# Performance work log

Measured on AMD Instinct MI355X. Metric: run time of the kernel, lower is better.

## Reference

```python
import jax, jax.numpy as jnp
import numpy as np

N, E, IN, H, C = 50000, 800000, 128, 256, 2
EPS = 1e-5


def setup_inputs() -> dict:
    key = jax.random.key(0)
    ks = jax.random.split(key, 12)
    inp = {
        "x": jax.random.normal(ks[0], (N, IN), jnp.float32),
        "edge_index": jax.random.randint(ks[1], (2, E), 0, N, jnp.int32),
        "w_nei0": jax.random.normal(ks[2], (IN, H), jnp.float32) * 0.05,
        "w_root0": jax.random.normal(ks[3], (IN, H), jnp.float32) * 0.05,
        "b0": jnp.zeros((H,), jnp.float32),
        "w_nei": jax.random.normal(ks[4], (2, H, H), jnp.float32) * 0.05,
        "w_root": jax.random.normal(ks[5], (2, H, H), jnp.float32) * 0.05,
        "b": jnp.zeros((2, H), jnp.float32),
        "bn_gamma": jnp.ones((3, H), jnp.float32),
        "bn_beta": jnp.zeros((3, H), jnp.float32),
        "bn_mean": jax.random.normal(ks[6], (3, H), jnp.float32) * 0.05,
        "bn_var": jnp.ones((3, H), jnp.float32),
        "w1": jax.random.normal(ks[7], (H, H // 2), jnp.float32) * 0.05,
        "b1": jnp.zeros((H // 2,), jnp.float32),
        "w2": jax.random.normal(ks[8], (H // 2, C), jnp.float32) * 0.05,
        "b2": jnp.zeros((C,), jnp.float32),
    }
    return inp


def _mean_aggregate(h, src, dst, inv_deg):
    # gather source-node features, scatter-sum to destinations, divide by degree
    agg = jax.ops.segment_sum(h[src], dst, num_segments=N)  # (N, d)
    return agg * inv_deg[:, None]


def _forward(x, edge_index, w_nei0, w_root0, b0, w_nei, w_root, b,
             bn_gamma, bn_beta, bn_mean, bn_var, w1, b1, w2, b2):
    src, dst = edge_index[0], edge_index[1]
    deg = jax.ops.segment_sum(jnp.ones((E,), x.dtype), dst, num_segments=N)
    inv_deg = 1.0 / jnp.maximum(deg, 1.0)

    h = x
    wn_list = [w_nei0, w_nei[0], w_nei[1]]
    wr_list = [w_root0, w_root[0], w_root[1]]
    bias_list = [b0, b[0], b[1]]
    for i in range(3):
        mean_nb = _mean_aggregate(h, src, dst, inv_deg)          # (N, d_in)
        h = mean_nb @ wn_list[i] + bias_list[i] + h @ wr_list[i]  # SAGEConv
        # BatchNorm1d (eval: running stats) + ReLU; dropout is identity in eval
        h = (h - bn_mean[i]) * jax.lax.rsqrt(bn_var[i] + EPS) * bn_gamma[i] + bn_beta[i]
        h = jax.nn.relu(h)

    h = jax.nn.relu(h @ w1 + b1)
    logits = h @ w2 + b2
    return jax.nn.log_softmax(logits, axis=1)


def reference(x, edge_index, w_nei0, w_root0, b0, w_nei, w_root, b,
              bn_gamma, bn_beta, bn_mean, bn_var, w1, b1, w2, b2):
    return _forward(x, edge_index, w_nei0, w_root0, b0, w_nei, w_root, b,
                    bn_gamma, bn_beta, bn_mean, bn_var, w1, b1, w2, b2)
```

## Files before the change

kernel.cpp:

```cpp
#include <hip/hip_runtime.h>
#include <hip/hip_fp16.h>

#define N_NODES 50000
#define N_EDGES 800000
#define DIM_IN 128
#define DIM_H 256

typedef _Float16 f16;
typedef _Float16 half8 __attribute__((ext_vector_type(8)));
typedef _Float16 f16x4 __attribute__((ext_vector_type(4)));
typedef _Float16 f16x2 __attribute__((ext_vector_type(2)));
typedef float f32x4 __attribute__((ext_vector_type(4)));
typedef unsigned int u32;

__device__ __forceinline__ void gload_lds16(const void* g, void* l) {
    __builtin_amdgcn_global_load_lds(
        (const __attribute__((address_space(1))) u32*)g,
        (__attribute__((address_space(3))) u32*)l,
        16, 0, 0);
}


__global__ void k_deg(const int* __restrict__ dst, int* __restrict__ deg) {
    int i = blockIdx.x * 256 + threadIdx.x;
    if (i < N_EDGES) atomicAdd(&deg[dst[i]], 1);
}

__global__ void k_scan1(const int* __restrict__ deg, int* __restrict__ row_start,
                        int* __restrict__ partials) {
    __shared__ int sm[256];
    int t = threadIdx.x;
    int i = blockIdx.x * 256 + t;
    int v = (i < N_NODES) ? deg[i] : 0;
    sm[t] = v;
    __syncthreads();
    for (int ofs = 1; ofs < 256; ofs <<= 1) {
        int add = (t >= ofs) ? sm[t - ofs] : 0;
        __syncthreads();
        sm[t] += add;
        __syncthreads();
    }
    if (i < N_NODES) row_start[i] = sm[t] - v;
    if (t == 255) partials[blockIdx.x] = sm[255];
}

__global__ void k_scan2(const int* __restrict__ partials, int* __restrict__ pscan, int nblk) {
    __shared__ int sm[256];
    int t = threadIdx.x;
    int v = (t < nblk) ? partials[t] : 0;
    sm[t] = v;
    __syncthreads();
    for (int ofs = 1; ofs < 256; ofs <<= 1) {
        int add = (t >= ofs) ? sm[t - ofs] : 0;
        __syncthreads();
        sm[t] += add;
        __syncthreads();
    }
    pscan[t] = sm[t] - v;
}

__global__ void k_scan3(const int* __restrict__ deg, int* __restrict__ row_start,
                        const int* __restrict__ pscan, float* __restrict__ inv_deg) {
    int i = blockIdx.x * 256 + threadIdx.x;
    if (i < N_NODES) {
        row_start[i] += pscan[blockIdx.x];
        int d = deg[i];
        inv_deg[i] = 1.0f / (float)(d > 1 ? d : 1);
        if (i == 0) row_start[N_NODES] = N_EDGES;
    }
}

__global__ void k_fill(const int* __restrict__ src, const int* __restrict__ dst,
                       const int* __restrict__ row_start, int* __restrict__ cursor,
                       int* __restrict__ csr) {
    int i = blockIdx.x * 256 + threadIdx.x;
    if (i < N_EDGES) {
        int d = dst[i];
        int p = atomicAdd(&cursor[d], 1);
        csr[row_start[d] + p] = src[i];
    }
}


__global__ void k_cvt_x(const float* __restrict__ x, f16* __restrict__ o) {
    int i = blockIdx.x * 256 + threadIdx.x;
    if (i < N_NODES * DIM_IN / 4) {
        float4 v = ((const float4*)x)[i];
        f16x4 h = {(f16)v.x, (f16)v.y, (f16)v.z, (f16)v.w};
        *(f16x4*)(o + (size_t)i * 4) = h;
    }
}

__global__ void k_tcvt(const float* __restrict__ W, f16* __restrict__ Wt, int K, int NN) {
    int t = blockIdx.x * 256 + threadIdx.x;
    if (t < K * NN) {
        int n = t / K, k = t - n * K;
        Wt[t] = (f16)W[(size_t)k * NN + n];
    }
}

__global__ void k_st(const float* __restrict__ b0, const float* __restrict__ bvec,
                     const float* __restrict__ gamma, const float* __restrict__ beta,
                     const float* __restrict__ mean, const float* __restrict__ var,
                     const float* __restrict__ b1, float* __restrict__ st) {
    int c = threadIdx.x;
    for (int layer = 0; layer < 3; layer++) {
        float bias = (layer == 0) ? b0[c] : bvec[(layer - 1) * DIM_H + c];
        float g = gamma[layer * DIM_H + c];
        float be = beta[layer * DIM_H + c];
        float mu = mean[layer * DIM_H + c];
        float va = var[layer * DIM_H + c];
        float s = g * rsqrtf(va + 1e-5f);
        st[layer * 512 + c] = s;
        st[layer * 512 + 256 + c] = (bias - mu) * s + be;
    }
    st[3 * 512 + c] = 1.0f;
    st[3 * 512 + 256 + c] = (c < 128) ? b1[c] : 0.0f;
}


template <int D>
__global__ void k_agg(const f16* __restrict__ h, const int* __restrict__ row_start,
                      const int* __restrict__ csr, const float* __restrict__ inv_deg,
                      f16* __restrict__ agg) {
    constexpr int V = D / 64;
    typedef _Float16 fvec __attribute__((ext_vector_type(V)));
    int wid = threadIdx.x >> 6;
    int lane = threadIdx.x & 63;
    int v = blockIdx.x * 4 + wid;
    if (v >= N_NODES) return;
    int e0 = row_start[v], e1 = row_start[v + 1];
    float acc[V];
#pragma unroll
    for (int j = 0; j < V; j++) acc[j] = 0.0f;

    const int li = lane & 15;
    for (int e = e0; e < e1; e += 16) {
        int ee = e + li;
        int idx = csr[ee < e1 ? ee : e1 - 1];
        int rem = e1 - e;
        fvec hv[16];
#pragma unroll
        for (int j = 0; j < 16; j++) {
            int s = __shfl(idx, j);
            hv[j] = *(const fvec*)(h + (size_t)s * D + lane * V);
        }
#pragma unroll
        for (int j = 0; j < 16; j++) {
            if (j < rem) {
#pragma unroll
                for (int q = 0; q < V; q++) acc[q] += (float)hv[j][q];
            }
        }
    }

    float sc = inv_deg[v];
    fvec o;
#pragma unroll
    for (int j = 0; j < V; j++) o[j] = (f16)(acc[j] * sc);
    *(fvec*)(agg + (size_t)v * D + lane * V) = o;
}


__global__ __launch_bounds__(256) void k_gemm(
    const f16* __restrict__ A1, int lda1, const f16* __restrict__ B1, int k1,
    const f16* __restrict__ A2, int lda2, const f16* __restrict__ B2, int k2,
    const float* __restrict__ sc, const float* __restrict__ sh,
    f16* __restrict__ out, int ldo, int M) {
    __shared__ f16 aT[128 * 32];
    __shared__ f16 bT[128 * 32];
    const int tid = threadIdx.x;
    const int lane = tid & 63;
    const int wid = tid >> 6;
    const int wm = wid >> 1, wn = wid & 1;
    const int m0 = blockIdx.x * 128;
    const int n0 = blockIdx.y * 128;
    f32x4 acc[4][4] = {};

    const int srow = tid >> 2;
    const int schunk = (tid & 3) ^ ((tid >> 3) & 3);
    const int ktot = k1 + k2;

    for (int kk = 0; kk < ktot; kk += 32) {
        const f16 *Ap, *Bp;
        int lda, ldb, kloc;
        if (kk < k1) { Ap = A1; Bp = B1; lda = lda1; ldb = k1; kloc = kk; }
        else         { Ap = A2; Bp = B2; lda = lda2; ldb = k2; kloc = kk - k1; }
#pragma unroll
        for (int hh = 0; hh < 2; hh++) {
            int r = hh * 64 + srow;
            int gm = m0 + r;
            gm = gm < M ? gm : M - 1;
            gload_lds16(Ap + (size_t)gm * lda + kloc + schunk * 8,
                        (char*)aT + hh * 4096 + tid * 16);
            gload_lds16(Bp + (size_t)(n0 + r) * ldb + kloc + schunk * 8,
                        (char*)bT + hh * 4096 + tid * 16);
        }
        __syncthreads();
        half8 af[4], bf[4];
#pragma unroll
        for (int mi = 0; mi < 4; mi++) {
            int row = wm * 64 + mi * 16 + (lane & 15);
            int ch = (lane >> 4) ^ ((row >> 1) & 3);
            af[mi] = *(const half8*)((const char*)aT + row * 64 + ch * 16);
        }
#pragma unroll
        for (int ni = 0; ni < 4; ni++) {
            int row = wn * 64 + ni * 16 + (lane & 15);
            int ch = (lane >> 4) ^ ((row >> 1) & 3);
            bf[ni] = *(const half8*)((const char*)bT + row * 64 + ch * 16);
        }
#pragma unroll
        for (int mi = 0; mi < 4; mi++)
#pragma unroll
            for (int ni = 0; ni < 4; ni++)
                acc[mi][ni] = __builtin_amdgcn_mfma_f32_16x16x32_f16(af[mi], bf[ni],
                                                                     acc[mi][ni], 0, 0, 0);
        __syncthreads();
    }

#pragma unroll
    for (int mi = 0; mi < 4; mi++) {
#pragma unroll
        for (int ni = 0; ni < 4; ni++) {
            int gcol = n0 + wn * 64 + ni * 16 + (lane & 15);
            float s = sc[gcol], t = sh[gcol];
#pragma unroll
            for (int r = 0; r < 4; r++) {
                int grow = m0 + wm * 64 + mi * 16 + (lane >> 4) * 4 + r;
                if (grow < M) {
                    float val = fmaxf(acc[mi][ni][r] * s + t, 0.0f);
                    out[(size_t)grow * ldo + gcol] = (f16)val;
                }
            }
        }
    }
}


__global__ void k_head2(const f16* __restrict__ h4, const float* __restrict__ w2,
                        const float* __restrict__ b2, float* __restrict__ out) {
    int wid = threadIdx.x >> 6, lane = threadIdx.x & 63;
    int row = blockIdx.x * 4 + wid;
    if (row >= N_NODES) return;
    f16x2 hv = *(const f16x2*)(h4 + (size_t)row * 128 + lane * 2);
    float4 w = *(const float4*)(w2 + lane * 4);
    float p0 = (float)hv[0] * w.x + (float)hv[1] * w.z;
    float p1 = (float)hv[0] * w.y + (float)hv[1] * w.w;
    for (int o = 32; o > 0; o >>= 1) {
        p0 += __shfl_xor(p0, o);
        p1 += __shfl_xor(p1, o);
    }
    if (lane == 0) {
        float l0 = p0 + b2[0], l1 = p1 + b2[1];
        float m = fmaxf(l0, l1);
        float lse = m + logf(expf(l0 - m) + expf(l1 - m));
        out[(size_t)row * 2] = l0 - lse;
        out[(size_t)row * 2 + 1] = l1 - lse;
    }
}


extern "C" void kernel_launch(void* const* d_in, const int* in_sizes, int n_in,
                              void* d_out, int out_size, void* d_ws, size_t ws_size,
                              hipStream_t stream) {
    const float* x     = (const float*)d_in[0];
    const int*   ei    = (const int*)d_in[1];
    const float* wn0   = (const float*)d_in[2];
    const float* wr0   = (const float*)d_in[3];
    const float* b0    = (const float*)d_in[4];
    const float* wn12  = (const float*)d_in[5];
    const float* wr12  = (const float*)d_in[6];
    const float* bvec  = (const float*)d_in[7];
    const float* gamma = (const float*)d_in[8];
    const float* beta  = (const float*)d_in[9];
    const float* mean  = (const float*)d_in[10];
    const float* var   = (const float*)d_in[11];
    const float* w1    = (const float*)d_in[12];
    const float* b1    = (const float*)d_in[13];
    const float* w2    = (const float*)d_in[14];
    const float* b2    = (const float*)d_in[15];
    const int* srcv = ei;
    const int* dstv = ei + N_EDGES;

    char* p = (char*)d_ws;
    auto alloc = [&](size_t bytes) {
        char* r = p;
        p += (bytes + 255) & ~(size_t)255;
        return r;
    };
    int*   deg       = (int*)alloc((size_t)N_NODES * 4);
    int*   row_start = (int*)alloc((size_t)(N_NODES + 1) * 4);
    int*   cursor    = (int*)alloc((size_t)N_NODES * 4);
    float* inv_deg   = (float*)alloc((size_t)N_NODES * 4);
    int*   partials  = (int*)alloc(256 * 4);
    int*   pscan     = (int*)alloc(256 * 4);
    int*   csr       = (int*)alloc((size_t)N_EDGES * 4);
    f16*   Wn0t      = (f16*)alloc(128 * 256 * 2);
    f16*   Wr0t      = (f16*)alloc(128 * 256 * 2);
    f16*   Wn1t      = (f16*)alloc(256 * 256 * 2);
    f16*   Wr1t      = (f16*)alloc(256 * 256 * 2);
    f16*   Wn2t      = (f16*)alloc(256 * 256 * 2);
    f16*   Wr2t      = (f16*)alloc(256 * 256 * 2);
    f16*   W1t       = (f16*)alloc(256 * 128 * 2);
    float* st        = (float*)alloc(4 * 512 * 4);
    f16*   hA        = (f16*)alloc((size_t)N_NODES * 256 * 2);
    f16*   hB        = (f16*)alloc((size_t)N_NODES * 256 * 2);
    f16*   agg       = (f16*)alloc((size_t)N_NODES * 256 * 2);

    hipMemsetAsync(deg, 0, (size_t)N_NODES * 4, stream);
    hipMemsetAsync(cursor, 0, (size_t)N_NODES * 4, stream);

    const int EB = (N_EDGES + 255) / 256;
    const int NBLK = (N_NODES + 255) / 256;
    k_deg<<<EB, 256, 0, stream>>>(dstv, deg);
    k_scan1<<<NBLK, 256, 0, stream>>>(deg, row_start, partials);
    k_scan2<<<1, 256, 0, stream>>>(partials, pscan, NBLK);
    k_scan3<<<NBLK, 256, 0, stream>>>(deg, row_start, pscan, inv_deg);
    k_fill<<<EB, 256, 0, stream>>>(srcv, dstv, row_start, cursor, csr);

    k_cvt_x<<<(N_NODES * DIM_IN / 4 + 255) / 256, 256, 0, stream>>>(x, hA);
    k_tcvt<<<128, 256, 0, stream>>>(wn0, Wn0t, 128, 256);
    k_tcvt<<<128, 256, 0, stream>>>(wr0, Wr0t, 128, 256);
    k_tcvt<<<256, 256, 0, stream>>>(wn12, Wn1t, 256, 256);
    k_tcvt<<<256, 256, 0, stream>>>(wn12 + 65536, Wn2t, 256, 256);
    k_tcvt<<<256, 256, 0, stream>>>(wr12, Wr1t, 256, 256);
    k_tcvt<<<256, 256, 0, stream>>>(wr12 + 65536, Wr2t, 256, 256);
    k_tcvt<<<128, 256, 0, stream>>>(w1, W1t, 256, 128);
    k_st<<<1, 256, 0, stream>>>(b0, bvec, gamma, beta, mean, var, b1, st);

    const int AB = (N_NODES + 3) / 4;
    dim3 g2((N_NODES + 127) / 128, 2), g1((N_NODES + 127) / 128, 1);

    k_agg<128><<<AB, 256, 0, stream>>>(hA, row_start, csr, inv_deg, agg);
    k_gemm<<<g2, 256, 0, stream>>>(agg, 128, Wn0t, 128, hA, 128, Wr0t, 128,
                                   st + 0, st + 256, hB, 256, N_NODES);
    k_agg<256><<<AB, 256, 0, stream>>>(hB, row_start, csr, inv_deg, agg);
    k_gemm<<<g2, 256, 0, stream>>>(agg, 256, Wn1t, 256, hB, 256, Wr1t, 256,
                                   st + 512, st + 768, hA, 256, N_NODES);
    k_agg<256><<<AB, 256, 0, stream>>>(hA, row_start, csr, inv_deg, agg);
    k_gemm<<<g2, 256, 0, stream>>>(agg, 256, Wn2t, 256, hA, 256, Wr2t, 256,
                                   st + 1024, st + 1280, hB, 256, N_NODES);
    k_gemm<<<g1, 256, 0, stream>>>(hB, 256, W1t, 256, (const f16*)nullptr, 0,
                                   (const f16*)nullptr, 0,
                                   st + 1536, st + 1792, agg, 128, N_NODES);
    k_head2<<<AB, 256, 0, stream>>>(agg, w2, b2, (float*)d_out);
}
```

Before: 398.1 us.

## Process two nodes per wave in aggregation and double-buffer GEMM LDS tiles

The aggregation kernel now has each wavefront gather neighbours for two destination nodes at once, which doubles the independent gather loads in flight to hide memory latency. The cost is more registers and wasted iterations when the two nodes' degrees differ. The GEMM now double-buffers its LDS tiles, issuing the next k-slice's global-to-LDS load before computing on the current one, and drops one barrier per iteration. This doubles LDS use, which may lower occupancy.

```diff
diff --git a/kernel.cpp b/kernel.cpp
--- a/kernel.cpp
+++ b/kernel.cpp
@@ -127,38 +127,70 @@
     typedef _Float16 fvec __attribute__((ext_vector_type(V)));
     int wid = threadIdx.x >> 6;
     int lane = threadIdx.x & 63;
-    int v = blockIdx.x * 4 + wid;
-    if (v >= N_NODES) return;
-    int e0 = row_start[v], e1 = row_start[v + 1];
-    float acc[V];
-#pragma unroll
-    for (int j = 0; j < V; j++) acc[j] = 0.0f;
+    int va = (blockIdx.x * 4 + wid) * 2;
+    if (va >= N_NODES) return;
+    int vb = va + 1;
+    bool hasB = vb < N_NODES;
+    int a0 = row_start[va], a1 = row_start[va + 1];
+    int b0 = hasB ? row_start[vb] : 0;
+    int b1 = hasB ? row_start[vb + 1] : 0;
+    float accA[V], accB[V];
+#pragma unroll
+    for (int j = 0; j < V; j++) { accA[j] = 0.0f; accB[j] = 0.0f; }
 
     const int li = lane & 15;
-    for (int e = e0; e < e1; e += 16) {
-        int ee = e + li;
-        int idx = csr[ee < e1 ? ee : e1 - 1];
-        int rem = e1 - e;
-        fvec hv[16];
+    int ea = a0, eb = b0;
+    while (ea < a1 || eb < b1) {
+        int pa = ea + li;
+        pa = pa < a1 ? pa : (a1 > a0 ? a1 - 1 : 0);
+        int pb = eb + li;
+        pb = pb < b1 ? pb : (b1 > b0 ? b1 - 1 : 0);
+        int idxa = csr[pa];
+        int idxb = csr[pb];
+        int remA = a1 - ea, remB = b1 - eb;
+        fvec hva[16], hvb[16];
 #pragma unroll
         for (int j = 0; j < 16; j++) {
-            int s = __shfl(idx, j);
-            hv[j] = *(const fvec*)(h + (size_t)s * D + lane * V);
+            int s = __shfl(idxa, j);
+            hva[j] = *(const fvec*)(h + (size_t)s * D + lane * V);
         }
 #pragma unroll
         for (int j = 0; j < 16; j++) {
-            if (j < rem) {
-#pragma unroll
-                for (int q = 0; q < V; q++) acc[q] += (float)hv[j][q];
+            int s = __shfl(idxb, j);
+            hvb[j] = *(const fvec*)(h + (size_t)s * D + lane * V);
+        }
+#pragma unroll
+        for (int j = 0; j < 16; j++) {
+            if (j < remA) {
+#pragma unroll
+                for (int q = 0; q < V; q++) accA[q] += (float)hva[j][q];
             }
         }
-    }
-
-    float sc = inv_deg[v];
-    fvec o;
-#pragma unroll
-    for (int j = 0; j < V; j++) o[j] = (f16)(acc[j] * sc);
-    *(fvec*)(agg + (size_t)v * D + lane * V) = o;
+#pragma unroll
+        for (int j = 0; j < 16; j++) {
+            if (j < remB) {
+#pragma unroll
+                for (int q = 0; q < V; q++) accB[q] += (float)hvb[j][q];
+            }
+        }
+        ea += 16;
+        eb += 16;
+    }
+
+    {
+        float sc = inv_deg[va];
+        fvec o;
+#pragma unroll
+        for (int j = 0; j < V; j++) o[j] = (f16)(accA[j] * sc);
+        *(fvec*)(agg + (size_t)va * D + lane * V) = o;
+    }
+    if (hasB) {
+        float sc = inv_deg[vb];
+        fvec o;
+#pragma unroll
+        for (int j = 0; j < V; j++) o[j] = (f16)(accB[j] * sc);
+        *(fvec*)(agg + (size_t)vb * D + lane * V) = o;
+    }
 }
 
 
@@ -167,8 +199,8 @@
     const f16* __restrict__ A2, int lda2, const f16* __restrict__ B2, int k2,
     const float* __restrict__ sc, const float* __restrict__ sh,
     f16* __restrict__ out, int ldo, int M) {
-    __shared__ f16 aT[128 * 32];
-    __shared__ f16 bT[128 * 32];
+    __shared__ f16 aT[2][128 * 32];
+    __shared__ f16 bT[2][128 * 32];
     const int tid = threadIdx.x;
     const int lane = tid & 63;
     const int wid = tid >> 6;
@@ -181,7 +213,7 @@
     const int schunk = (tid & 3) ^ ((tid >> 3) & 3);
     const int ktot = k1 + k2;
 
-    for (int kk = 0; kk < ktot; kk += 32) {
+    auto stage = [&](int buf, int kk) {
         const f16 *Ap, *Bp;
         int lda, ldb, kloc;
         if (kk < k1) { Ap = A1; Bp = B1; lda = lda1; ldb = k1; kloc = kk; }
@@ -192,23 +224,25 @@
             int gm = m0 + r;
             gm = gm < M ? gm : M - 1;
             gload_lds16(Ap + (size_t)gm * lda + kloc + schunk * 8,
-                        (char*)aT + hh * 4096 + tid * 16);
+                        (char*)&aT[buf][0] + hh * 4096 + tid * 16);
             gload_lds16(Bp + (size_t)(n0 + r) * ldb + kloc + schunk * 8,
-                        (char*)bT + hh * 4096 + tid * 16);
-        }
-        __syncthreads();
+                        (char*)&bT[buf][0] + hh * 4096 + tid * 16);
+        }
+    };
+
+    auto compute = [&](int buf) {
         half8 af[4], bf[4];
 #pragma unroll
         for (int mi = 0; mi < 4; mi++) {
             int row = wm * 64 + mi * 16 + (lane & 15);
             int ch = (lane >> 4) ^ ((row >> 1) & 3);
-            af[mi] = *(const half8*)((const char*)aT + row * 64 + ch * 16);
+            af[mi] = *(const half8*)((const char*)&aT[buf][0] + row * 64 + ch * 16);
         }
 #pragma unroll
         for (int ni = 0; ni < 4; ni++) {
             int row = wn * 64 + ni * 16 + (lane & 15);
             int ch = (lane >> 4) ^ ((row >> 1) & 3);
-            bf[ni] = *(const half8*)((const char*)bT + row * 64 + ch * 16);
+            bf[ni] = *(const half8*)((const char*)&bT[buf][0] + row * 64 + ch * 16);
         }
 #pragma unroll
         for (int mi = 0; mi < 4; mi++)
@@ -216,8 +250,18 @@
             for (int ni = 0; ni < 4; ni++)
                 acc[mi][ni] = __builtin_amdgcn_mfma_f32_16x16x32_f16(af[mi], bf[ni],
                                                                      acc[mi][ni], 0, 0, 0);
-        __syncthreads();
-    }
+    };
+
+    stage(0, 0);
+    __syncthreads();
+    int cur = 0;
+    for (int kk = 32; kk < ktot; kk += 32) {
+        stage(cur ^ 1, kk);
+        compute(cur);
+        __syncthreads();
+        cur ^= 1;
+    }
+    compute(cur);
 
 #pragma unroll
     for (int mi = 0; mi < 4; mi++) {
@@ -329,16 +373,17 @@
     k_tcvt<<<128, 256, 0, stream>>>(w1, W1t, 256, 128);
     k_st<<<1, 256, 0, stream>>>(b0, bvec, gamma, beta, mean, var, b1, st);
 
-    const int AB = (N_NODES + 3) / 4;
+    const int AB2 = (N_NODES + 7) / 8;
+    const int AB  = (N_NODES + 3) / 4;
     dim3 g2((N_NODES + 127) / 128, 2), g1((N_NODES + 127) / 128, 1);
 
-    k_agg<128><<<AB, 256, 0, stream>>>(hA, row_start, csr, inv_deg, agg);
+    k_agg<128><<<AB2, 256, 0, stream>>>(hA, row_start, csr, inv_deg, agg);
     k_gemm<<<g2, 256, 0, stream>>>(agg, 128, Wn0t, 128, hA, 128, Wr0t, 128,
                                    st + 0, st + 256, hB, 256, N_NODES);
-    k_agg<256><<<AB, 256, 0, stream>>>(hB, row_start, csr, inv_deg, agg);
+    k_agg<256><<<AB2, 256, 0, stream>>>(hB, row_start, csr, inv_deg, agg);
     k_gemm<<<g2, 256, 0, stream>>>(agg, 256, Wn1t, 256, hB, 256, Wr1t, 256,
                                    st + 512, st + 768, hA, 256, N_NODES);
-    k_agg<256><<<AB, 256, 0, stream>>>(hA, row_start, csr, inv_deg, agg);
+    k_agg<256><<<AB2, 256, 0, stream>>>(hA, row_start, csr, inv_deg, agg);
     k_gemm<<<g2, 256, 0, stream>>>(agg, 256, Wn2t, 256, hA, 256, Wr2t, 256,
                                    st + 1024, st + 1280, hB, 256, N_NODES);
     k_gemm<<<g1, 256, 0, stream>>>(hB, 256, W1t, 256, (const f16*)nullptr, 0,
```

New measurement: 417.9 us. 5.0% more time.

## Triple-buffer GEMM LDS loads and switch to 32x32x16 MFMA tiles

Applied to the files above, without the earlier changes.

The GEMM kernel now keeps three LDS stages and issues global-to-LDS loads two k-steps ahead, waiting on vmcnt instead of a full sync per step, so load latency can overlap MFMA work. It also replaces the 16x16x32 MFMA grid with 32x32x16 instructions, which cuts the number of LDS fragment reads per MFMA. The cost is more LDS per block (48KB), which may lower occupancy, plus a redundant final prefetch of the last step.

```diff
diff --git a/kernel.cpp b/kernel.cpp
--- a/kernel.cpp
+++ b/kernel.cpp
@@ -11,6 +11,7 @@
 typedef _Float16 f16x4 __attribute__((ext_vector_type(4)));
 typedef _Float16 f16x2 __attribute__((ext_vector_type(2)));
 typedef float f32x4 __attribute__((ext_vector_type(4)));
+typedef float f32x16 __attribute__((ext_vector_type(16)));
 typedef unsigned int u32;
 
 __device__ __forceinline__ void gload_lds16(const void* g, void* l) {
@@ -167,21 +168,22 @@
     const f16* __restrict__ A2, int lda2, const f16* __restrict__ B2, int k2,
     const float* __restrict__ sc, const float* __restrict__ sh,
     f16* __restrict__ out, int ldo, int M) {
-    __shared__ f16 aT[128 * 32];
-    __shared__ f16 bT[128 * 32];
+    __shared__ f16 aT[3][128 * 32];
+    __shared__ f16 bT[3][128 * 32];
     const int tid = threadIdx.x;
     const int lane = tid & 63;
     const int wid = tid >> 6;
     const int wm = wid >> 1, wn = wid & 1;
     const int m0 = blockIdx.x * 128;
     const int n0 = blockIdx.y * 128;
-    f32x4 acc[4][4] = {};
+    f32x16 acc[2][2] = {};
 
     const int srow = tid >> 2;
     const int schunk = (tid & 3) ^ ((tid >> 3) & 3);
     const int ktot = k1 + k2;
-
-    for (int kk = 0; kk < ktot; kk += 32) {
+    const int nsteps = ktot >> 5;
+
+    auto stage = [&](int buf, int kk) {
         const f16 *Ap, *Bp;
         int lda, ldb, kloc;
         if (kk < k1) { Ap = A1; Bp = B1; lda = lda1; ldb = k1; kloc = kk; }
@@ -192,44 +194,64 @@
             int gm = m0 + r;
             gm = gm < M ? gm : M - 1;
             gload_lds16(Ap + (size_t)gm * lda + kloc + schunk * 8,
-                        (char*)aT + hh * 4096 + tid * 16);
+                        (char*)&aT[buf][0] + hh * 4096 + tid * 16);
             gload_lds16(Bp + (size_t)(n0 + r) * ldb + kloc + schunk * 8,
-                        (char*)bT + hh * 4096 + tid * 16);
+                        (char*)&bT[buf][0] + hh * 4096 + tid * 16);
         }
-        __syncthreads();
-        half8 af[4], bf[4];
-#pragma unroll
-        for (int mi = 0; mi < 4; mi++) {
-            int row = wm * 64 + mi * 16 + (lane & 15);
-            int ch = (lane >> 4) ^ ((row >> 1) & 3);
-            af[mi] = *(const half8*)((const char*)aT + row * 64 + ch * 16);
-        }
-#pragma unroll
-        for (int ni = 0; ni < 4; ni++) {
-            int row = wn * 64 + ni * 16 + (lane & 15);
-            int ch = (lane >> 4) ^ ((row >> 1) & 3);
-            bf[ni] = *(const half8*)((const char*)bT + row * 64 + ch * 16);
-        }
-#pragma unroll
-        for (int mi = 0; mi < 4; mi++)
-#pragma unroll
-            for (int ni = 0; ni < 4; ni++)
-                acc[mi][ni] = __builtin_amdgcn_mfma_f32_16x16x32_f16(af[mi], bf[ni],
-                                                                     acc[mi][ni], 0, 0, 0);
-        __syncthreads();
-    }
-
-#pragma unroll
-    for (int mi = 0; mi < 4; mi++) {
-#pragma unroll
-        for (int ni = 0; ni < 4; ni++) {
-            int gcol = n0 + wn * 64 + ni * 16 + (lane & 15);
+    };
+
+    auto compute = [&](int buf) {
+        half8 af[2][2], bf[2][2];
+#pragma unroll
+        for (int mi = 0; mi < 2; mi++)
+#pragma unroll
+            for (int ks = 0; ks < 2; ks++) {
+                int row = wm * 64 + mi * 32 + (lane & 31);
+                int ch = (ks * 2 + (lane >> 5)) ^ ((row >> 1) & 3);
+                af[mi][ks] = *(const half8*)((const char*)&aT[buf][0] + row * 64 + ch * 16);
+            }
+#pragma unroll
+        for (int ni = 0; ni < 2; ni++)
+#pragma unroll
+            for (int ks = 0; ks < 2; ks++) {
+                int row = wn * 64 + ni * 32 + (lane & 31);
+                int ch = (ks * 2 + (lane >> 5)) ^ ((row >> 1) & 3);
+                bf[ni][ks] = *(const half8*)((const char*)&bT[buf][0] + row * 64 + ch * 16);
+            }
+#pragma unroll
+        for (int mi = 0; mi < 2; mi++)
+#pragma unroll
+            for (int ni = 0; ni < 2; ni++)
+#pragma unroll
+                for (int ks = 0; ks < 2; ks++)
+                    acc[mi][ni] = __builtin_amdgcn_mfma_f32_32x32x16_f16(
+                        af[mi][ks], bf[ni][ks], acc[mi][ni], 0, 0, 0);
+    };
+
+    stage(0, 0);
+    stage(1, 32);
+    for (int i = 0; i < nsteps; i++) {
+        asm volatile("s_waitcnt vmcnt(4)" ::: "memory");
+        __builtin_amdgcn_s_barrier();
+        __builtin_amdgcn_sched_barrier(0);
+        int pk = i + 2 < nsteps ? i + 2 : nsteps - 1;
+        stage((i + 2) % 3, pk * 32);
+        __builtin_amdgcn_sched_barrier(0);
+        compute(i % 3);
+    }
+
+#pragma unroll
+    for (int mi = 0; mi < 2; mi++) {
+#pragma unroll
+        for (int ni = 0; ni < 2; ni++) {
+            int gcol = n0 + wn * 64 + ni * 32 + (lane & 31);
             float s = sc[gcol], t = sh[gcol];
-#pragma unroll
-            for (int r = 0; r < 4; r++) {
-                int grow = m0 + wm * 64 + mi * 16 + (lane >> 4) * 4 + r;
+            int rbase = m0 + wm * 64 + mi * 32 + 4 * (lane >> 5);
+#pragma unroll
+            for (int reg = 0; reg < 16; reg++) {
+                int grow = rbase + (reg & 3) + 8 * (reg >> 2);
                 if (grow < M) {
-                    float val = fmaxf(acc[mi][ni][r] * s + t, 0.0f);
+                    float val = fmaxf(acc[mi][ni][reg] * s + t, 0.0f);
                     out[(size_t)grow * ldo + gcol] = (f16)val;
                 }
             }
```

New measurement: 421.0 us. 5.8% more time.
